# Performance work log

Hardware: AMD Instinct MI355X
Metric: run time of the kernel (lower is better)

Reference implementation:

```python
import jax, jax.numpy as jnp
import numpy as np

N_NODES = 100000
NEG_SLOPE = 0.01  # F.leaky_relu default


def _gin_mean_layer(x, src, dst):
    """DGL GINConv(aggregator='mean', apply_func=None, eps=0, activation=leaky_relu).
    out = leaky_relu((1+eps)*x + mean_{in-neighbors} x_src), nodes with no in-edges get mean=0.
    """
    msg_sum = jax.ops.segment_sum(x[src], dst, num_segments=N_NODES)  # [N, D]
    deg = jax.ops.segment_sum(jnp.ones(src.shape, dtype=x.dtype), dst, num_segments=N_NODES)  # [N]
    mean = msg_sum / jnp.maximum(deg, 1.0)[:, None]
    return jax.nn.leaky_relu(x + mean, negative_slope=NEG_SLOPE)


def setup_inputs() -> dict:
    key = jax.random.key(0)
    k0, k1, k2, k3, k4 = jax.random.split(key, 5)
    n_edges = 640000
    d = 128
    return {
        "node_features": jax.random.normal(k0, (N_NODES, d), dtype=jnp.float32),
        "edges1_src": jax.random.randint(k1, (n_edges,), 0, N_NODES, dtype=jnp.int64),
        "edges1_dst": jax.random.randint(k2, (n_edges,), 0, N_NODES, dtype=jnp.int64),
        "edges2_src": jax.random.randint(k3, (n_edges,), 0, N_NODES, dtype=jnp.int64),
        "edges2_dst": jax.random.randint(k4, (n_edges,), 0, N_NODES, dtype=jnp.int64),
    }


def reference(node_features, edges1_src, edges1_dst, edges2_src, edges2_dst):
    h_AC1 = _gin_mean_layer(node_features, edges1_src, edges1_dst)
    h_CA1 = _gin_mean_layer(node_features, edges2_src, edges2_dst)
    h = jnp.concatenate((h_AC1, h_CA1), axis=1)  # [N, 2D]
    h_AC2 = _gin_mean_layer(h, edges1_src, edges1_dst)
    h_CA2 = _gin_mean_layer(h, edges2_src, edges2_dst)
    return jnp.concatenate((h_AC2, h_CA2), axis=1)  # [N, 4D]
```

## Files before the change

### kernel.cpp

```cpp
#include <hip/hip_runtime.h>

#define N_NODES 100000
#define NEG 0.01f
#define CAP 32

__device__ __forceinline__ float lrelu(float v) { return v > 0.f ? v : NEG * v; }

__device__ __forceinline__ unsigned int f2bf(float f) {
    unsigned int x = __float_as_uint(f);
    return (x + 0x7fffu + ((x >> 16) & 1u)) >> 16;
}
__device__ __forceinline__ unsigned int pack2bf(float lo, float hi) {
    return f2bf(lo) | (f2bf(hi) << 16);
}
__device__ __forceinline__ float bf_lo(unsigned int u) { return __uint_as_float(u << 16); }
__device__ __forceinline__ float bf_hi(unsigned int u) { return __uint_as_float(u & 0xffff0000u); }

__global__ void build_slots(const int* __restrict__ src, const int* __restrict__ dst, int E,
                            int* __restrict__ deg, int* __restrict__ slots) {
    int i = blockIdx.x * blockDim.x + threadIdx.x;
    if (i >= E) return;
    int d = dst[i];
    int pos = atomicAdd(&deg[d], 1);
    if (pos < CAP) slots[d * CAP + pos] = src[i];
}

__global__ void convert_x(const float* __restrict__ x, unsigned int* __restrict__ xb) {
    int i = blockIdx.x * blockDim.x + threadIdx.x;
    if (i >= N_NODES * 32) return;
    float4 v = ((const float4*)x)[i];
    uint2 p;
    p.x = pack2bf(v.x, v.y);
    p.y = pack2bf(v.z, v.w);
    ((uint2*)xb)[i] = p;
}

__global__ void __launch_bounds__(256) layer1(
        const unsigned int* __restrict__ xb,
        const int* __restrict__ deg1, const int* __restrict__ slots1,
        const int* __restrict__ deg2, const int* __restrict__ slots2,
        unsigned int* __restrict__ hb) {
    int gid = blockIdx.x * blockDim.x + threadIdx.x;
    int n = gid >> 6;
    int lane = gid & 63;
    if (n >= N_NODES) return;

    unsigned int xu = xb[(size_t)n * 64 + lane];
    float x0 = bf_lo(xu), x1 = bf_hi(xu);

    int d1 = deg1[n];
    int d2 = deg2[n];
    int m1 = min(d1, CAP);
    int m2 = min(d2, CAP);
    int my1 = (lane < m1) ? slots1[n * CAP + lane] : 0;
    int my2 = (lane < m2) ? slots2[n * CAP + lane] : 0;

    float s1a = 0.f, s1b = 0.f, s2a = 0.f, s2b = 0.f;
    for (int j = 0; j < m1; ++j) {
        int s = __shfl(my1, j);
        unsigned int u = xb[(size_t)s * 64 + lane];
        s1a += bf_lo(u); s1b += bf_hi(u);
    }
    for (int j = 0; j < m2; ++j) {
        int s = __shfl(my2, j);
        unsigned int u = xb[(size_t)s * 64 + lane];
        s2a += bf_lo(u); s2b += bf_hi(u);
    }
    float r1 = 1.f / (float)max(d1, 1);
    float r2 = 1.f / (float)max(d2, 1);
    hb[(size_t)n * 128 + lane]      = pack2bf(lrelu(x0 + s1a * r1), lrelu(x1 + s1b * r1));
    hb[(size_t)n * 128 + 64 + lane] = pack2bf(lrelu(x0 + s2a * r2), lrelu(x1 + s2b * r2));
}

__global__ void __launch_bounds__(256) layer2(
        const unsigned int* __restrict__ hb,
        const int* __restrict__ deg1, const int* __restrict__ slots1,
        const int* __restrict__ deg2, const int* __restrict__ slots2,
        float* __restrict__ out) {
    int gid = blockIdx.x * blockDim.x + threadIdx.x;
    int n = gid >> 6;
    int lane = gid & 63;
    if (n >= N_NODES) return;

    const uint2* hrows = (const uint2*)hb;
    uint2 hu = hrows[(size_t)n * 64 + lane];
    float h0 = bf_lo(hu.x), h1 = bf_hi(hu.x), h2 = bf_lo(hu.y), h3 = bf_hi(hu.y);

    int d1 = deg1[n];
    int d2 = deg2[n];
    int m1 = min(d1, CAP);
    int m2 = min(d2, CAP);
    int my1 = (lane < m1) ? slots1[n * CAP + lane] : 0;
    int my2 = (lane < m2) ? slots2[n * CAP + lane] : 0;

    float a0 = 0.f, a1 = 0.f, a2 = 0.f, a3 = 0.f;
    float b0 = 0.f, b1 = 0.f, b2 = 0.f, b3 = 0.f;
    for (int j = 0; j < m1; ++j) {
        int s = __shfl(my1, j);
        uint2 u = hrows[(size_t)s * 64 + lane];
        a0 += bf_lo(u.x); a1 += bf_hi(u.x); a2 += bf_lo(u.y); a3 += bf_hi(u.y);
    }
    for (int j = 0; j < m2; ++j) {
        int s = __shfl(my2, j);
        uint2 u = hrows[(size_t)s * 64 + lane];
        b0 += bf_lo(u.x); b1 += bf_hi(u.x); b2 += bf_lo(u.y); b3 += bf_hi(u.y);
    }
    float r1 = 1.f / (float)max(d1, 1);
    float r2 = 1.f / (float)max(d2, 1);
    float4 A, B;
    A.x = lrelu(h0 + a0 * r1); A.y = lrelu(h1 + a1 * r1);
    A.z = lrelu(h2 + a2 * r1); A.w = lrelu(h3 + a3 * r1);
    B.x = lrelu(h0 + b0 * r2); B.y = lrelu(h1 + b1 * r2);
    B.z = lrelu(h2 + b2 * r2); B.w = lrelu(h3 + b3 * r2);
    float4* ob = (float4*)out;
    ob[(size_t)n * 128 + lane]      = A;
    ob[(size_t)n * 128 + 64 + lane] = B;
}

extern "C" void kernel_launch(void* const* d_in, const int* in_sizes, int n_in,
                              void* d_out, int out_size, void* d_ws, size_t ws_size,
                              hipStream_t stream) {
    const float* x = (const float*)d_in[0];
    const int* e1s = (const int*)d_in[1];
    const int* e1d = (const int*)d_in[2];
    const int* e2s = (const int*)d_in[3];
    const int* e2d = (const int*)d_in[4];
    const int E1 = in_sizes[1];
    const int E2 = in_sizes[3];
    float* out = (float*)d_out;

    int* deg1   = (int*)d_ws;
    int* deg2   = deg1 + N_NODES;
    int* slots1 = deg2 + N_NODES;
    int* slots2 = slots1 + (size_t)N_NODES * CAP;
    unsigned int* xb = (unsigned int*)(slots2 + (size_t)N_NODES * CAP);
    unsigned int* hb = xb + (size_t)N_NODES * 64;

    hipMemsetAsync(deg1, 0, 2ull * N_NODES * sizeof(int), stream);

    build_slots<<<(E1 + 255) / 256, 256, 0, stream>>>(e1s, e1d, E1, deg1, slots1);
    build_slots<<<(E2 + 255) / 256, 256, 0, stream>>>(e2s, e2d, E2, deg2, slots2);
    convert_x<<<(N_NODES * 32 + 255) / 256, 256, 0, stream>>>(x, xb);

    int blocks = (N_NODES + 3) / 4;
    layer1<<<blocks, 256, 0, stream>>>(xb, deg1, slots1, deg2, slots2, hb);
    layer2<<<blocks, 256, 0, stream>>>(hb, deg1, slots1, deg2, slots2, out);
}
```

Measured before the change: 527.8 us.

## Gather multiple neighbors per wavefront with 16-byte loads and cross-group reduction

Layer kernels now split each 64-lane wavefront into groups that each gather a different neighbor row with 16-byte uint4 loads, then combine the partial sums with cross-lane xor shuffles. This raises memory-level parallelism and halves the serial loop trip count per node. The two slot-building kernels are merged into a single launch, convert_x uses wider vectors, and the output is written with nontemporal stores. The cost is extra shuffle reductions and idle lanes during the final writes.

```diff
diff --git a/kernel.cpp b/kernel.cpp
--- a/kernel.cpp
+++ b/kernel.cpp
@@ -4,6 +4,8 @@
 #define NEG 0.01f
 #define CAP 32
 
+typedef float f4v __attribute__((ext_vector_type(4)));
+
 __device__ __forceinline__ float lrelu(float v) { return v > 0.f ? v : NEG * v; }
 
 __device__ __forceinline__ unsigned int f2bf(float f) {
@@ -16,105 +18,181 @@
 __device__ __forceinline__ float bf_lo(unsigned int u) { return __uint_as_float(u << 16); }
 __device__ __forceinline__ float bf_hi(unsigned int u) { return __uint_as_float(u & 0xffff0000u); }
 
-__global__ void build_slots(const int* __restrict__ src, const int* __restrict__ dst, int E,
-                            int* __restrict__ deg, int* __restrict__ slots) {
+__device__ __forceinline__ void unpack8(uint4 u, float* f) {
+    f[0] = bf_lo(u.x); f[1] = bf_hi(u.x);
+    f[2] = bf_lo(u.y); f[3] = bf_hi(u.y);
+    f[4] = bf_lo(u.z); f[5] = bf_hi(u.z);
+    f[6] = bf_lo(u.w); f[7] = bf_hi(u.w);
+}
+
+__global__ void build_both(const int* __restrict__ s1, const int* __restrict__ d1a, int E1,
+                           const int* __restrict__ s2, const int* __restrict__ d2a, int E2,
+                           int* __restrict__ deg1, int* __restrict__ slots1,
+                           int* __restrict__ deg2, int* __restrict__ slots2) {
     int i = blockIdx.x * blockDim.x + threadIdx.x;
-    if (i >= E) return;
-    int d = dst[i];
-    int pos = atomicAdd(&deg[d], 1);
-    if (pos < CAP) slots[d * CAP + pos] = src[i];
-}
-
-__global__ void convert_x(const float* __restrict__ x, unsigned int* __restrict__ xb) {
+    if (i < E1) {
+        int d = d1a[i];
+        int pos = atomicAdd(&deg1[d], 1);
+        if (pos < CAP) slots1[d * CAP + pos] = s1[i];
+    }
+    int k = i - E1;
+    if (k >= 0 && k < E2) {
+        int d = d2a[k];
+        int pos = atomicAdd(&deg2[d], 1);
+        if (pos < CAP) slots2[d * CAP + pos] = s2[k];
+    }
+}
+
+__global__ void convert_x(const float4* __restrict__ x, uint4* __restrict__ xb) {
     int i = blockIdx.x * blockDim.x + threadIdx.x;
-    if (i >= N_NODES * 32) return;
-    float4 v = ((const float4*)x)[i];
-    uint2 p;
-    p.x = pack2bf(v.x, v.y);
-    p.y = pack2bf(v.z, v.w);
-    ((uint2*)xb)[i] = p;
+    if (i >= N_NODES * 16) return;
+    float4 v0 = x[2 * i];
+    float4 v1 = x[2 * i + 1];
+    uint4 p;
+    p.x = pack2bf(v0.x, v0.y);
+    p.y = pack2bf(v0.z, v0.w);
+    p.z = pack2bf(v1.x, v1.y);
+    p.w = pack2bf(v1.z, v1.w);
+    xb[i] = p;
 }
 
 __global__ void __launch_bounds__(256) layer1(
-        const unsigned int* __restrict__ xb,
+        const uint4* __restrict__ x4,
         const int* __restrict__ deg1, const int* __restrict__ slots1,
         const int* __restrict__ deg2, const int* __restrict__ slots2,
-        unsigned int* __restrict__ hb) {
+        uint4* __restrict__ h4) {
     int gid = blockIdx.x * blockDim.x + threadIdx.x;
     int n = gid >> 6;
+    if (n >= N_NODES) return;
     int lane = gid & 63;
-    if (n >= N_NODES) return;
-
-    unsigned int xu = xb[(size_t)n * 64 + lane];
-    float x0 = bf_lo(xu), x1 = bf_hi(xu);
-
-    int d1 = deg1[n];
-    int d2 = deg2[n];
-    int m1 = min(d1, CAP);
-    int m2 = min(d2, CAP);
+    int t = lane & 15;
+    int g = lane >> 4;
+
+    uint4 xv = x4[(size_t)n * 16 + t];
+
+    int d1 = deg1[n], d2 = deg2[n];
+    int m1 = min(d1, CAP), m2 = min(d2, CAP);
     int my1 = (lane < m1) ? slots1[n * CAP + lane] : 0;
     int my2 = (lane < m2) ? slots2[n * CAP + lane] : 0;
 
-    float s1a = 0.f, s1b = 0.f, s2a = 0.f, s2b = 0.f;
-    for (int j = 0; j < m1; ++j) {
+    float a[8] = {0.f, 0.f, 0.f, 0.f, 0.f, 0.f, 0.f, 0.f};
+    float b[8] = {0.f, 0.f, 0.f, 0.f, 0.f, 0.f, 0.f, 0.f};
+
+    for (int j0 = 0; j0 < m1; j0 += 4) {
+        int j = j0 + g;
         int s = __shfl(my1, j);
-        unsigned int u = xb[(size_t)s * 64 + lane];
-        s1a += bf_lo(u); s1b += bf_hi(u);
-    }
-    for (int j = 0; j < m2; ++j) {
+        uint4 u = make_uint4(0u, 0u, 0u, 0u);
+        if (j < m1) u = x4[(size_t)s * 16 + t];
+        float f[8]; unpack8(u, f);
+        #pragma unroll
+        for (int i = 0; i < 8; ++i) a[i] += f[i];
+    }
+    for (int j0 = 0; j0 < m2; j0 += 4) {
+        int j = j0 + g;
         int s = __shfl(my2, j);
-        unsigned int u = xb[(size_t)s * 64 + lane];
-        s2a += bf_lo(u); s2b += bf_hi(u);
-    }
+        uint4 u = make_uint4(0u, 0u, 0u, 0u);
+        if (j < m2) u = x4[(size_t)s * 16 + t];
+        float f[8]; unpack8(u, f);
+        #pragma unroll
+        for (int i = 0; i < 8; ++i) b[i] += f[i];
+    }
+
+    #pragma unroll
+    for (int i = 0; i < 8; ++i) {
+        a[i] += __shfl_xor(a[i], 16);
+        a[i] += __shfl_xor(a[i], 32);
+        b[i] += __shfl_xor(b[i], 16);
+        b[i] += __shfl_xor(b[i], 32);
+    }
+
+    float xf[8]; unpack8(xv, xf);
     float r1 = 1.f / (float)max(d1, 1);
     float r2 = 1.f / (float)max(d2, 1);
-    hb[(size_t)n * 128 + lane]      = pack2bf(lrelu(x0 + s1a * r1), lrelu(x1 + s1b * r1));
-    hb[(size_t)n * 128 + 64 + lane] = pack2bf(lrelu(x0 + s2a * r2), lrelu(x1 + s2b * r2));
+
+    if (g == 0) {
+        uint4 o;
+        o.x = pack2bf(lrelu(xf[0] + a[0] * r1), lrelu(xf[1] + a[1] * r1));
+        o.y = pack2bf(lrelu(xf[2] + a[2] * r1), lrelu(xf[3] + a[3] * r1));
+        o.z = pack2bf(lrelu(xf[4] + a[4] * r1), lrelu(xf[5] + a[5] * r1));
+        o.w = pack2bf(lrelu(xf[6] + a[6] * r1), lrelu(xf[7] + a[7] * r1));
+        h4[(size_t)n * 32 + t] = o;
+    } else if (g == 1) {
+        uint4 o;
+        o.x = pack2bf(lrelu(xf[0] + b[0] * r2), lrelu(xf[1] + b[1] * r2));
+        o.y = pack2bf(lrelu(xf[2] + b[2] * r2), lrelu(xf[3] + b[3] * r2));
+        o.z = pack2bf(lrelu(xf[4] + b[4] * r2), lrelu(xf[5] + b[5] * r2));
+        o.w = pack2bf(lrelu(xf[6] + b[6] * r2), lrelu(xf[7] + b[7] * r2));
+        h4[(size_t)n * 32 + 16 + t] = o;
+    }
 }
 
 __global__ void __launch_bounds__(256) layer2(
-        const unsigned int* __restrict__ hb,
+        const uint4* __restrict__ h4,
         const int* __restrict__ deg1, const int* __restrict__ slots1,
         const int* __restrict__ deg2, const int* __restrict__ slots2,
-        float* __restrict__ out) {
+        float4* __restrict__ out4) {
     int gid = blockIdx.x * blockDim.x + threadIdx.x;
     int n = gid >> 6;
+    if (n >= N_NODES) return;
     int lane = gid & 63;
-    if (n >= N_NODES) return;
-
-    const uint2* hrows = (const uint2*)hb;
-    uint2 hu = hrows[(size_t)n * 64 + lane];
-    float h0 = bf_lo(hu.x), h1 = bf_hi(hu.x), h2 = bf_lo(hu.y), h3 = bf_hi(hu.y);
-
-    int d1 = deg1[n];
-    int d2 = deg2[n];
-    int m1 = min(d1, CAP);
-    int m2 = min(d2, CAP);
+    int t = lane & 31;
+    int g = lane >> 5;
+
+    uint4 hv = h4[(size_t)n * 32 + t];
+
+    int d1 = deg1[n], d2 = deg2[n];
+    int m1 = min(d1, CAP), m2 = min(d2, CAP);
     int my1 = (lane < m1) ? slots1[n * CAP + lane] : 0;
     int my2 = (lane < m2) ? slots2[n * CAP + lane] : 0;
 
-    float a0 = 0.f, a1 = 0.f, a2 = 0.f, a3 = 0.f;
-    float b0 = 0.f, b1 = 0.f, b2 = 0.f, b3 = 0.f;
-    for (int j = 0; j < m1; ++j) {
+    float a[8] = {0.f, 0.f, 0.f, 0.f, 0.f, 0.f, 0.f, 0.f};
+    float b[8] = {0.f, 0.f, 0.f, 0.f, 0.f, 0.f, 0.f, 0.f};
+
+    for (int j0 = 0; j0 < m1; j0 += 2) {
+        int j = j0 + g;
         int s = __shfl(my1, j);
-        uint2 u = hrows[(size_t)s * 64 + lane];
-        a0 += bf_lo(u.x); a1 += bf_hi(u.x); a2 += bf_lo(u.y); a3 += bf_hi(u.y);
-    }
-    for (int j = 0; j < m2; ++j) {
+        uint4 u = make_uint4(0u, 0u, 0u, 0u);
+        if (j < m1) u = h4[(size_t)s * 32 + t];
+        float f[8]; unpack8(u, f);
+        #pragma unroll
+        for (int i = 0; i < 8; ++i) a[i] += f[i];
+    }
+    for (int j0 = 0; j0 < m2; j0 += 2) {
+        int j = j0 + g;
         int s = __shfl(my2, j);
-        uint2 u = hrows[(size_t)s * 64 + lane];
-        b0 += bf_lo(u.x); b1 += bf_hi(u.x); b2 += bf_lo(u.y); b3 += bf_hi(u.y);
-    }
+        uint4 u = make_uint4(0u, 0u, 0u, 0u);
+        if (j < m2) u = h4[(size_t)s * 32 + t];
+        float f[8]; unpack8(u, f);
+        #pragma unroll
+        for (int i = 0; i < 8; ++i) b[i] += f[i];
+    }
+
+    #pragma unroll
+    for (int i = 0; i < 8; ++i) {
+        a[i] += __shfl_xor(a[i], 32);
+        b[i] += __shfl_xor(b[i], 32);
+    }
+
+    float hf[8]; unpack8(hv, hf);
     float r1 = 1.f / (float)max(d1, 1);
     float r2 = 1.f / (float)max(d2, 1);
-    float4 A, B;
-    A.x = lrelu(h0 + a0 * r1); A.y = lrelu(h1 + a1 * r1);
-    A.z = lrelu(h2 + a2 * r1); A.w = lrelu(h3 + a3 * r1);
-    B.x = lrelu(h0 + b0 * r2); B.y = lrelu(h1 + b1 * r2);
-    B.z = lrelu(h2 + b2 * r2); B.w = lrelu(h3 + b3 * r2);
-    float4* ob = (float4*)out;
-    ob[(size_t)n * 128 + lane]      = A;
-    ob[(size_t)n * 128 + 64 + lane] = B;
+
+    f4v* ob = (f4v*)out4;
+    if (g == 0) {
+        f4v A0 = {lrelu(hf[0] + a[0] * r1), lrelu(hf[1] + a[1] * r1),
+                  lrelu(hf[2] + a[2] * r1), lrelu(hf[3] + a[3] * r1)};
+        f4v A1 = {lrelu(hf[4] + a[4] * r1), lrelu(hf[5] + a[5] * r1),
+                  lrelu(hf[6] + a[6] * r1), lrelu(hf[7] + a[7] * r1)};
+        __builtin_nontemporal_store(A0, &ob[(size_t)n * 128 + 2 * t]);
+        __builtin_nontemporal_store(A1, &ob[(size_t)n * 128 + 2 * t + 1]);
+    } else {
+        f4v B0 = {lrelu(hf[0] + b[0] * r2), lrelu(hf[1] + b[1] * r2),
+                  lrelu(hf[2] + b[2] * r2), lrelu(hf[3] + b[3] * r2)};
+        f4v B1 = {lrelu(hf[4] + b[4] * r2), lrelu(hf[5] + b[5] * r2),
+                  lrelu(hf[6] + b[6] * r2), lrelu(hf[7] + b[7] * r2)};
+        __builtin_nontemporal_store(B0, &ob[(size_t)n * 128 + 64 + 2 * t]);
+        __builtin_nontemporal_store(B1, &ob[(size_t)n * 128 + 64 + 2 * t + 1]);
+    }
 }
 
 extern "C" void kernel_launch(void* const* d_in, const int* in_sizes, int n_in,
@@ -138,11 +216,14 @@
 
     hipMemsetAsync(deg1, 0, 2ull * N_NODES * sizeof(int), stream);
 
-    build_slots<<<(E1 + 255) / 256, 256, 0, stream>>>(e1s, e1d, E1, deg1, slots1);
-    build_slots<<<(E2 + 255) / 256, 256, 0, stream>>>(e2s, e2d, E2, deg2, slots2);
-    convert_x<<<(N_NODES * 32 + 255) / 256, 256, 0, stream>>>(x, xb);
+    build_both<<<(E1 + E2 + 255) / 256, 256, 0, stream>>>(
+        e1s, e1d, E1, e2s, e2d, E2, deg1, slots1, deg2, slots2);
+    convert_x<<<(N_NODES * 16 + 255) / 256, 256, 0, stream>>>(
+        (const float4*)x, (uint4*)xb);
 
     int blocks = (N_NODES + 3) / 4;
-    layer1<<<blocks, 256, 0, stream>>>(xb, deg1, slots1, deg2, slots2, hb);
-    layer2<<<blocks, 256, 0, stream>>>(hb, deg1, slots1, deg2, slots2, out);
-}
+    layer1<<<blocks, 256, 0, stream>>>(
+        (const uint4*)xb, deg1, slots1, deg2, slots2, (uint4*)hb);
+    layer2<<<blocks, 256, 0, stream>>>(
+        (const uint4*)hb, deg1, slots1, deg2, slots2, (float4*)out);
+}
```

Result: no change. 520.2 us (-1.4%).
